# Kernel optimization log

Hardware: AMD Instinct MI355X
Metric: run time of the kernel (lower is better)

The kernel has to match this reference:

```python
import jax, jax.numpy as jnp
import numpy as np

N = 100000   # nodes per type
E = 500000   # edges per edge type
HID = 128    # hidden_channels
H = 4        # heads
D = HID // H # head dim = 32
L = 2        # layers
T = 2        # node types: 0=user, 1=item
R = 2        # edge types: 0=user->item, 1=item->user


def setup_inputs() -> dict:
    key = jax.random.key(0)
    ks = jax.random.split(key, 16)
    s = jnp.float32(0.05)
    f32 = jnp.float32
    return {
        "x_user": jax.random.normal(ks[0], (N, HID), f32),
        "x_item": jax.random.normal(ks[1], (N, HID), f32),
        "W_in": jax.random.normal(ks[2], (T, HID, HID), f32) * s,
        "b_in": jnp.zeros((T, HID), f32),
        "Wk": jax.random.normal(ks[3], (L, T, HID, HID), f32) * s,
        "bk": jnp.zeros((L, T, HID), f32),
        "Wq": jax.random.normal(ks[4], (L, T, HID, HID), f32) * s,
        "bq": jnp.zeros((L, T, HID), f32),
        "Wv": jax.random.normal(ks[5], (L, T, HID, HID), f32) * s,
        "bv": jnp.zeros((L, T, HID), f32),
        "a_rel": jax.random.normal(ks[6], (L, R, H, D, D), f32) * s,
        "m_rel": jax.random.normal(ks[7], (L, R, H, D, D), f32) * s,
        "p_rel": jnp.ones((L, R, H), f32),
        "Wo": jax.random.normal(ks[8], (L, T, HID, HID), f32) * s,
        "bo": jnp.zeros((L, T, HID), f32),
        "skip": jnp.zeros((L, T), f32),
        "edge_ui": jax.random.randint(ks[9], (2, E), 0, N, dtype=jnp.int32),
        "edge_iu": jax.random.randint(ks[10], (2, E), 0, N, dtype=jnp.int32),
    }


def _seg_softmax(logits, seg, n):
    # numerically stable softmax over edges grouped by destination node
    m = jax.ops.segment_max(logits, seg, num_segments=n)            # [N,H]
    m = jnp.where(jnp.isfinite(m), m, jnp.float32(0.0))
    e = jnp.exp(logits - m[seg])                                    # [E,H]
    z = jax.ops.segment_sum(e, seg, num_segments=n)                 # [N,H]
    return e / (z[seg] + jnp.float32(1e-16))


def reference(x_user, x_item, W_in, b_in, Wk, bk, Wq, bq, Wv, bv,
              a_rel, m_rel, p_rel, Wo, bo, skip, edge_ui, edge_iu):
    scale = jnp.float32(1.0 / np.sqrt(D))
    # per-node-type input linear + relu (lin_dict)
    h = [jax.nn.relu(x_user @ W_in[0] + b_in[0]),
         jax.nn.relu(x_item @ W_in[1] + b_in[1])]
    # (edge_type_id, src_type, dst_type, edge_index)
    etypes = [(0, 0, 1, edge_ui), (1, 1, 0, edge_iu)]
    for l in range(L):
        k = [(h[t] @ Wk[l, t] + bk[l, t]).reshape(N, H, D) for t in range(T)]
        q = [(h[t] @ Wq[l, t] + bq[l, t]).reshape(N, H, D) for t in range(T)]
        v = [(h[t] @ Wv[l, t] + bv[l, t]).reshape(N, H, D) for t in range(T)]
        agg = [jnp.zeros((N, H, D), h[0].dtype) for _ in range(T)]
        for r, st, dt, e in etypes:
            src, dst = e[0], e[1]
            # relation-specific transforms applied on node table (N < E)
            k_r = jnp.einsum('nhd,hde->nhe', k[st], a_rel[l, r])
            v_r = jnp.einsum('nhd,hde->nhe', v[st], m_rel[l, r])
            logits = jnp.sum(q[dt][dst] * k_r[src], axis=-1) * p_rel[l, r] * scale  # [E,H]
            alpha = _seg_softmax(logits, dst, N)                                    # [E,H]
            msg = alpha[:, :, None] * v_r[src]                                      # [E,H,D]
            agg[dt] = agg[dt] + jax.ops.segment_sum(msg, dst, num_segments=N)
        h_new = []
        for t in range(T):
            out = agg[t].reshape(N, HID)
            a = jax.nn.gelu(out, approximate=False) @ Wo[l, t] + bo[l, t]
            beta = jax.nn.sigmoid(skip[l, t])
            hn = beta * a + (1.0 - beta) * h[t]
            if l > 0:  # model-level residual (i > 0 in torch code)
                hn = hn + h[t]
            h_new.append(hn)
        h = h_new
    return jnp.stack(h)  # [T, N, HID]
```

## Files before the change

kernel.cpp:

```cpp
#include <hip/hip_runtime.h>
#include <stdint.h>
#include <stdio.h>

#define NN 100000
#define NE 500000
#define HID 128
#define NH 4
#define HD 32
#define LL 2
#define SCANB 1024
#define NB ((NN + SCANB - 1) / SCANB)

typedef unsigned short u16;
typedef unsigned char u8;
typedef unsigned int u32;
typedef __attribute__((ext_vector_type(8))) short bfrag;
typedef __attribute__((ext_vector_type(4))) float f32x4;
typedef __attribute__((ext_vector_type(2))) float f32x2;

__device__ __forceinline__ float b2f(u32 lo16) {
  union { u32 u; float f; } c; c.u = lo16; return c.f;
}
__device__ __forceinline__ u16 f2b(float f) {
  union { float f; u32 u; } c; c.f = f;
  u32 u = c.u;
  u32 r = (u + 0x7FFFu + ((u >> 16) & 1u)) >> 16;
  return (u16)r;
}
__device__ __forceinline__ float geluf(float x) {
  return 0.5f * x * (1.0f + erff(x * 0.70710678118654752f));
}
__device__ __forceinline__ void up8(uint4 a, float* f) {
  f[0] = b2f(a.x << 16); f[1] = b2f(a.x & 0xFFFF0000u);
  f[2] = b2f(a.y << 16); f[3] = b2f(a.y & 0xFFFF0000u);
  f[4] = b2f(a.z << 16); f[5] = b2f(a.z & 0xFFFF0000u);
  f[6] = b2f(a.w << 16); f[7] = b2f(a.w & 0xFFFF0000u);
}

__global__ __launch_bounds__(256) void csr_count(const int* __restrict__ e0,
                                                 const int* __restrict__ e1,
                                                 int* __restrict__ deg) {
  int r = blockIdx.y;
  const int* edges = r ? e1 : e0;
  int e = blockIdx.x * 256 + threadIdx.x;
  if (e < NE) atomicAdd(&deg[(size_t)r * NN + edges[NE + e]], 1);
}

__global__ __launch_bounds__(SCANB) void scan1(const int* __restrict__ deg,
                                               int* __restrict__ rp,
                                               int* __restrict__ bsum) {
  __shared__ int ls[SCANB];
  int r = blockIdx.y;
  int t = threadIdx.x;
  int g = blockIdx.x * SCANB + t;
  int v = (g < NN) ? deg[(size_t)r * NN + g] : 0;
  ls[t] = v;
  __syncthreads();
#pragma unroll
  for (int off = 1; off < SCANB; off <<= 1) {
    int u = (t >= off) ? ls[t - off] : 0;
    __syncthreads();
    ls[t] += u;
    __syncthreads();
  }
  if (g < NN) rp[(size_t)r * (NN + 1) + g] = ls[t] - v;
  if (t == SCANB - 1) bsum[r * NB + blockIdx.x] = ls[t];
}

__global__ __launch_bounds__(128) void scan2(const int* __restrict__ bsum,
                                             int* __restrict__ boff) {
  __shared__ int ls[128];
  int r = blockIdx.y;
  int t = threadIdx.x;
  int v = (t < NB) ? bsum[r * NB + t] : 0;
  ls[t] = v;
  __syncthreads();
#pragma unroll
  for (int off = 1; off < 128; off <<= 1) {
    int u = (t >= off) ? ls[t - off] : 0;
    __syncthreads();
    ls[t] += u;
    __syncthreads();
  }
  if (t < NB) boff[r * NB + t] = ls[t] - v;
}

__global__ __launch_bounds__(SCANB) void scan3(int* __restrict__ rp,
                                               int* __restrict__ cursor,
                                               const int* __restrict__ boff) {
  int r = blockIdx.y;
  int g = blockIdx.x * SCANB + threadIdx.x;
  if (g < NN) {
    int v = rp[(size_t)r * (NN + 1) + g] + boff[r * NB + blockIdx.x];
    rp[(size_t)r * (NN + 1) + g] = v;
    cursor[(size_t)r * NN + g] = v;
  }
  if (g == 0) rp[(size_t)r * (NN + 1) + NN] = NE;
}

__global__ __launch_bounds__(256) void csr_fill(const int* __restrict__ e0,
                                                const int* __restrict__ e1,
                                                int* __restrict__ cursor,
                                                int* __restrict__ s0,
                                                int* __restrict__ s1) {
  int r = blockIdx.y;
  const int* edges = r ? e1 : e0;
  int* srcs = r ? s1 : s0;
  int e = blockIdx.x * 256 + threadIdx.x;
  if (e < NE) {
    int pos = atomicAdd(&cursor[(size_t)r * NN + edges[NE + e]], 1);
    srcs[pos] = edges[e];
  }
}

__global__ __launch_bounds__(256) void hist_deg(const int* __restrict__ rp,
                                                int* __restrict__ hist) {
  __shared__ int lh[64];
  int r = blockIdx.y;
  if (threadIdx.x < 64) lh[threadIdx.x] = 0;
  __syncthreads();
  int d = blockIdx.x * 256 + threadIdx.x;
  if (d < NN) {
    const int* rowptr = rp + (size_t)r * (NN + 1);
    int dg = rowptr[d + 1] - rowptr[d];
    atomicAdd(&lh[dg < 63 ? dg : 63], 1);
  }
  __syncthreads();
  if (threadIdx.x < 64 && lh[threadIdx.x])
    atomicAdd(&hist[r * 64 + threadIdx.x], lh[threadIdx.x]);
}

__global__ __launch_bounds__(64) void scan_hist(const int* __restrict__ hist,
                                                int* __restrict__ hcur) {
  __shared__ int ls[64];
  int r = blockIdx.y;
  int t = threadIdx.x;
  int v = hist[r * 64 + t];
  ls[t] = v;
  __syncthreads();
#pragma unroll
  for (int off = 1; off < 64; off <<= 1) {
    int u = (t >= off) ? ls[t - off] : 0;
    __syncthreads();
    ls[t] += u;
    __syncthreads();
  }
  hcur[r * 64 + t] = ls[t] - v;
}

__global__ __launch_bounds__(256) void scatter_deg(const int* __restrict__ rp,
                                                   int* __restrict__ hcur,
                                                   int* __restrict__ o0,
                                                   int* __restrict__ o1) {
  __shared__ int lh[64];
  __shared__ int lbase[64];
  int r = blockIdx.y;
  int* order = r ? o1 : o0;
  if (threadIdx.x < 64) lh[threadIdx.x] = 0;
  __syncthreads();
  int d = blockIdx.x * 256 + threadIdx.x;
  int dg = 0, rank = 0;
  if (d < NN) {
    const int* rowptr = rp + (size_t)r * (NN + 1);
    dg = rowptr[d + 1] - rowptr[d];
    if (dg > 63) dg = 63;
    rank = atomicAdd(&lh[dg], 1);
  }
  __syncthreads();
  if (threadIdx.x < 64)
    lbase[threadIdx.x] = lh[threadIdx.x] ? atomicAdd(&hcur[r * 64 + threadIdx.x], lh[threadIdx.x]) : 0;
  __syncthreads();
  if (d < NN) order[lbase[dg] + rank] = d;
}

__global__ __launch_bounds__(256) void prep_wT(const float* __restrict__ src, size_t srcStride,
                                               u16* __restrict__ dst, size_t dstStride,
                                               const float* __restrict__ bsrc, int bsStride,
                                               float* __restrict__ bdst, int bdStride,
                                               const float* __restrict__ p_rel_q) {
  int m = blockIdx.y;
  const float* S = src + (size_t)m * srcStride;
  u16* D = dst + (size_t)m * dstStride;
  int idx = blockIdx.x * 256 + threadIdx.x;
  int k = idx >> 7, n = idx & 127;
  float v = S[idx];
  if (p_rel_q != nullptr) {
    int l = m >> 1, t = m & 1;
    v *= p_rel_q[((l << 1) | (1 - t)) * NH + (n >> 5)] * 0.17677669529663687f;
  }
  D[(size_t)n * HID + k] = f2b(v);
  if (bsrc != nullptr && blockIdx.x == 0 && threadIdx.x < HID) {
    int col = threadIdx.x;
    float bvv = bsrc[(size_t)m * bsStride + col];
    if (p_rel_q != nullptr) {
      int l = m >> 1, t = m & 1;
      bvv *= p_rel_q[((l << 1) | (1 - t)) * NH + (col >> 5)] * 0.17677669529663687f;
    }
    bdst[(size_t)m * bdStride + col] = bvv;
  }
}

__global__ __launch_bounds__(256) void combine_all(
    const float* __restrict__ Wk, const float* __restrict__ bk,
    const float* __restrict__ Wv, const float* __restrict__ bv,
    const float* __restrict__ a_rel, const float* __restrict__ m_rel,
    u16* __restrict__ wqkvT, float* __restrict__ bqkv) {
  int l = blockIdx.z;
  int t = blockIdx.y >> 1, which = blockIdx.y & 1;
  const float* W  = (which == 0 ? Wk : Wv) + (size_t)(l * 2 + t) * HID * HID;
  const float* b  = (which == 0 ? bk : bv) + (size_t)(l * 2 + t) * HID;
  const float* Ar = (which == 0 ? a_rel : m_rel) + (size_t)(l * 2 + t) * NH * HD * HD;
  u16* Wd = wqkvT + ((size_t)(l * 2 + t) * 3 + 1 + which) * HID * HID;
  float* bd = bqkv + ((size_t)(l * 2 + t) * 3 + 1 + which) * HID;
  int idx = blockIdx.x * 256 + threadIdx.x;
  int i = idx >> 7, col = idx & 127;
  int h = col >> 5, e = col & 31;
  {
    const float* ap = Ar + h * HD * HD + e;
    const float* wp = W + (size_t)i * HID + h * HD;
    float s = 0.f;
#pragma unroll
    for (int d = 0; d < HD; ++d) s += wp[d] * ap[d * HD];
    Wd[(size_t)col * HID + i] = f2b(s);
  }
  if (blockIdx.x == 0 && threadIdx.x < HID) {
    int col2 = threadIdx.x, h2 = col2 >> 5, e2 = col2 & 31;
    const float* ap = Ar + h2 * HD * HD + e2;
    const float* bp = b + h2 * HD;
    float s = 0.f;
#pragma unroll
    for (int d = 0; d < HD; ++d) s += bp[d] * ap[d * HD];
    bd[col2] = s;
  }
}

__global__ __launch_bounds__(256) void qkv_gemm(
    const u16* __restrict__ h0, const u16* __restrict__ h1,
    const u16* __restrict__ WT,
    const float* __restrict__ bias,
    u16* __restrict__ q0, u16* __restrict__ q1,
    u8* __restrict__ k0, u8* __restrict__ k1,
    u8* __restrict__ v0, u8* __restrict__ v1, int gb) {
  __shared__ __align__(16) u16 sW[3 * HID * HID];
  const int t = blockIdx.x >= gb;
  const int bx = t ? blockIdx.x - gb : blockIdx.x;
  const u16* A = t ? h1 : h0;
  const u16* Wg = WT + (size_t)t * 3 * HID * HID;
  const float* bs = bias + (size_t)t * 3 * HID;
  u16* Oq = t ? q1 : q0;
  u8* Ok = t ? k1 : k0;
  u8* Ov = t ? v1 : v0;

  const int lane = threadIdx.x & 63;
  const int wid = threadIdx.x >> 6;
  const int l16 = lane & 15, g = lane >> 4;
  const int rbase = bx * 128 + wid * 32;

  bfrag af[2][4];
  int rowA[2];
#pragma unroll
  for (int rt = 0; rt < 2; ++rt) {
    int row = rbase + rt * 16 + l16;
    rowA[rt] = row;
    int rl = row < NN ? row : NN - 1;
    const bfrag* ap = (const bfrag*)(A + (size_t)rl * HID);
#pragma unroll
    for (int ks = 0; ks < 4; ++ks) af[rt][ks] = ap[ks * 4 + g];
  }

#pragma unroll
  for (int m = 0; m < 3; ++m) {
#pragma unroll
    for (int j = 0; j < 8; ++j) {
      int ins = wid * 8 + j;
      int o16 = ins * 64 + lane;
      int row = o16 >> 4, ch = o16 & 15;
      const u16* src = Wg + (size_t)m * HID * HID + (size_t)row * HID + ((ch ^ (row & 7)) << 3);
      u16* dst = sW + (size_t)m * HID * HID + (size_t)ins * 512;
      __builtin_amdgcn_global_load_lds(
          (const __attribute__((address_space(1))) unsigned int*)src,
          (__attribute__((address_space(3))) unsigned int*)dst, 16, 0, 0);
    }
  }
  __syncthreads();

#pragma unroll
  for (int m = 0; m < 3; ++m) {
    f32x4 acc[2][8];
#pragma unroll
    for (int rt = 0; rt < 2; ++rt)
#pragma unroll
      for (int ct = 0; ct < 8; ++ct) acc[rt][ct] = (f32x4){0.f, 0.f, 0.f, 0.f};
#pragma unroll
    for (int ct = 0; ct < 8; ++ct) {
      int row = ct * 16 + l16;
      bfrag wf[4];
#pragma unroll
      for (int ks = 0; ks < 4; ++ks)
        wf[ks] = *(const bfrag*)&sW[(size_t)m * HID * HID + (size_t)row * HID +
                                    (((ks * 4 + g) ^ (row & 7)) << 3)];
#pragma unroll
      for (int ks = 0; ks < 4; ++ks)
#pragma unroll
        for (int rt = 0; rt < 2; ++rt)
          acc[rt][ct] = __builtin_amdgcn_mfma_f32_16x16x32_bf16(wf[ks], af[rt][ks],
                                                                acc[rt][ct], 0, 0, 0);
    }
#pragma unroll
    for (int rt = 0; rt < 2; ++rt) {
      int row = rowA[rt];
      if (row >= NN) continue;
#pragma unroll
      for (int ct = 0; ct < 8; ++ct) {
        int nc = ct * 16 + g * 4;
        const float4 bb = *(const float4*)(bs + m * HID + nc);
        float o0 = acc[rt][ct][0] + bb.x;
        float o1 = acc[rt][ct][1] + bb.y;
        float o2 = acc[rt][ct][2] + bb.z;
        float o3 = acc[rt][ct][3] + bb.w;
        if (m == 0) {
          u32 lo = (u32)f2b(o0) | ((u32)f2b(o1) << 16);
          u32 hi = (u32)f2b(o2) | ((u32)f2b(o3) << 16);
          *(uint2*)(Oq + (size_t)row * HID + nc) = make_uint2(lo, hi);
        } else {
          u8* O8 = (m == 1) ? Ok : Ov;
          u32 pk = __builtin_amdgcn_cvt_pk_fp8_f32(o0, o1, 0u, false);
          pk = __builtin_amdgcn_cvt_pk_fp8_f32(o2, o3, pk, true);
          *(u32*)(O8 + (size_t)row * HID + nc) = pk;
        }
      }
    }
  }
}

template <int NMAT, bool RELU, bool SKIP, bool FP8KV, bool AF32>
__global__ __launch_bounds__(256) void mfgemm(
    const void* __restrict__ A0, const void* __restrict__ A1, int M, int gb,
    const u16* __restrict__ WT, size_t wtStride,
    const float* __restrict__ bias, size_t biasStride,
    u16* __restrict__ O00, u16* __restrict__ O01, u16* __restrict__ O02,
    u16* __restrict__ O10, u16* __restrict__ O11, u16* __restrict__ O12,
    float* __restrict__ Of0, float* __restrict__ Of1,
    const u16* __restrict__ hp0, const u16* __restrict__ hp1,
    const float* __restrict__ skipP, int resflag) {
  __shared__ __align__(16) u16 sW[HID * HID];
  const int t = blockIdx.x >= gb;
  const int bx = t ? blockIdx.x - gb : blockIdx.x;
  const void* A = t ? A1 : A0;
  const u16* Wg = WT + (size_t)t * wtStride;
  const float* bs = bias + (size_t)t * biasStride;
  u16* Os[3];
  Os[0] = t ? O10 : O00; Os[1] = t ? O11 : O01; Os[2] = t ? O12 : O02;
  float* Of = t ? Of1 : Of0;
  const u16* hprev = t ? hp1 : hp0;

  const int lane = threadIdx.x & 63;
  const int wid = threadIdx.x >> 6;
  const int l16 = lane & 15, g = lane >> 4;
  const int rbase = bx * 128 + wid * 32;

  float beta = 0.f;
  if (SKIP) beta = 1.f / (1.f + __expf(-skipP[t]));

  auto stageW = [&](int m) {
    const u16* Wm = Wg + (size_t)m * HID * HID;
#pragma unroll
    for (int j = 0; j < 8; ++j) {
      int ins = wid * 8 + j;
      int o16 = ins * 64 + lane;
      int row = o16 >> 4, ch = o16 & 15;
      const u16* src = Wm + (size_t)row * HID + ((ch ^ (row & 7)) << 3);
      u16* dst = sW + (size_t)ins * 512;
      __builtin_amdgcn_global_load_lds(
          (const __attribute__((address_space(1))) unsigned int*)src,
          (__attribute__((address_space(3))) unsigned int*)dst, 16, 0, 0);
    }
  };

  bfrag af[2][4];
  int rowA[2];
#pragma unroll
  for (int rt = 0; rt < 2; ++rt) {
    int row = rbase + rt * 16 + l16;
    rowA[rt] = row;
    int rl = row < M ? row : M - 1;
    if (AF32) {
      const float* apf = (const float*)A + (size_t)rl * HID;
#pragma unroll
      for (int ks = 0; ks < 4; ++ks) {
        float4 u0 = *(const float4*)(apf + (ks * 4 + g) * 8);
        float4 u1 = *(const float4*)(apf + (ks * 4 + g) * 8 + 4);
        union { u16 s[8]; bfrag b; } pk;
        pk.s[0] = f2b(u0.x); pk.s[1] = f2b(u0.y); pk.s[2] = f2b(u0.z); pk.s[3] = f2b(u0.w);
        pk.s[4] = f2b(u1.x); pk.s[5] = f2b(u1.y); pk.s[6] = f2b(u1.z); pk.s[7] = f2b(u1.w);
        af[rt][ks] = pk.b;
      }
    } else {
      const bfrag* ap = (const bfrag*)A + (size_t)rl * (HID / 8);
#pragma unroll
      for (int ks = 0; ks < 4; ++ks) af[rt][ks] = ap[ks * 4 + g];
    }
  }

  stageW(0);
  __syncthreads();

#pragma unroll
  for (int m = 0; m < NMAT; ++m) {
    f32x4 acc[2][8];
#pragma unroll
    for (int rt = 0; rt < 2; ++rt)
#pragma unroll
      for (int ct = 0; ct < 8; ++ct) acc[rt][ct] = (f32x4){0.f, 0.f, 0.f, 0.f};
#pragma unroll
    for (int ct = 0; ct < 8; ++ct) {
      int row = ct * 16 + l16;
      bfrag wf[4];
#pragma unroll
      for (int ks = 0; ks < 4; ++ks)
        wf[ks] = *(const bfrag*)&sW[(size_t)row * HID + (((ks * 4 + g) ^ (row & 7)) << 3)];
#pragma unroll
      for (int ks = 0; ks < 4; ++ks)
#pragma unroll
        for (int rt = 0; rt < 2; ++rt)
          acc[rt][ct] = __builtin_amdgcn_mfma_f32_16x16x32_bf16(wf[ks], af[rt][ks],
                                                                acc[rt][ct], 0, 0, 0);
    }
    if (m + 1 < NMAT) {
      __syncthreads();
      stageW(m + 1);
    }
    u16* Ob = Os[m];
#pragma unroll
    for (int rt = 0; rt < 2; ++rt) {
      int row = rowA[rt];
      if (row >= M) continue;
#pragma unroll
      for (int ct = 0; ct < 8; ++ct) {
        int nc = ct * 16 + g * 4;
        const float4 bb = *(const float4*)(bs + m * HID + nc);
        float o0 = acc[rt][ct][0] + bb.x;
        float o1 = acc[rt][ct][1] + bb.y;
        float o2 = acc[rt][ct][2] + bb.z;
        float o3 = acc[rt][ct][3] + bb.w;
        if (RELU) {
          o0 = fmaxf(o0, 0.f); o1 = fmaxf(o1, 0.f);
          o2 = fmaxf(o2, 0.f); o3 = fmaxf(o3, 0.f);
        }
        if (SKIP) {
          uint2 hh2 = *(const uint2*)(hprev + (size_t)row * HID + nc);
          float h0 = b2f(hh2.x << 16), h1 = b2f(hh2.x & 0xFFFF0000u);
          float h2 = b2f(hh2.y << 16), h3 = b2f(hh2.y & 0xFFFF0000u);
          o0 = beta * o0 + (1.f - beta) * h0;
          o1 = beta * o1 + (1.f - beta) * h1;
          o2 = beta * o2 + (1.f - beta) * h2;
          o3 = beta * o3 + (1.f - beta) * h3;
          if (resflag) { o0 += h0; o1 += h1; o2 += h2; o3 += h3; }
        }
        if (FP8KV && m >= 1) {
          u32 pk = __builtin_amdgcn_cvt_pk_fp8_f32(o0, o1, 0u, false);
          pk = __builtin_amdgcn_cvt_pk_fp8_f32(o2, o3, pk, true);
          *(u32*)((u8*)Ob + (size_t)row * HID + nc) = pk;
        } else {
          if (Ob != nullptr) {
            u32 lo = (u32)f2b(o0) | ((u32)f2b(o1) << 16);
            u32 hi = (u32)f2b(o2) | ((u32)f2b(o3) << 16);
            *(uint2*)(Ob + (size_t)row * HID + nc) = make_uint2(lo, hi);
          }
          if (NMAT == 1 && Of != nullptr) {
            *(float4*)(Of + (size_t)row * HID + nc) = make_float4(o0, o1, o2, o3);
          }
        }
      }
    }
    if (m + 1 < NMAT) __syncthreads();
  }
}

__global__ __launch_bounds__(256) void agg_csr(
    const int* __restrict__ rp0, const int* __restrict__ ss0, const int* __restrict__ od0,
    const u16* __restrict__ q0, const u8* __restrict__ k0,
    const u8* __restrict__ v0, u16* __restrict__ o0,
    const int* __restrict__ rp1, const int* __restrict__ ss1, const int* __restrict__ od1,
    const u16* __restrict__ q1, const u8* __restrict__ k1,
    const u8* __restrict__ v1, u16* __restrict__ o1, int agb) {
  const int r = blockIdx.x >= agb;
  const int bx = r ? blockIdx.x - agb : blockIdx.x;
  int i = bx * 256 + threadIdx.x;
  if (i >= NN * NH) return;
  const int* rowptr = r ? rp1 : rp0;
  const int* srcs = r ? ss1 : ss0;
  const int* order = r ? od1 : od0;
  const u16* qT = r ? q1 : q0;
  const u8* kT = r ? k1 : k0;
  const u8* vT = r ? v1 : v0;
  u16* aggb = r ? o1 : o0;

  int dst = order[i >> 2], h = i & 3;
  float qv[HD];
  {
    const uint4* qp = (const uint4*)(qT + (size_t)dst * HID + h * HD);
#pragma unroll
    for (int j = 0; j < 4; ++j) up8(qp[j], qv + j * 8);
  }
  float acc[HD];
#pragma unroll
  for (int j = 0; j < HD; ++j) acc[j] = 0.f;
  float z = 0.f;
  int b = rowptr[dst], e2 = rowptr[dst + 1];
  for (int idx = b; idx < e2; ++idx) {
    int src = srcs[idx];
    const uint4* kp = (const uint4*)(kT + (size_t)src * HID + h * HD);
    const uint4* vp = (const uint4*)(vT + (size_t)src * HID + h * HD);
    uint4 ka0 = kp[0], ka1 = kp[1];
    uint4 va0 = vp[0], va1 = vp[1];
    u32 kw[8] = {ka0.x, ka0.y, ka0.z, ka0.w, ka1.x, ka1.y, ka1.z, ka1.w};
    u32 vw[8] = {va0.x, va0.y, va0.z, va0.w, va1.x, va1.y, va1.z, va1.w};
    float s = 0.f;
#pragma unroll
    for (int j = 0; j < 8; ++j) {
      f32x2 p0 = __builtin_amdgcn_cvt_pk_f32_fp8(kw[j], false);
      f32x2 p1 = __builtin_amdgcn_cvt_pk_f32_fp8(kw[j], true);
      s += qv[4 * j] * p0.x + qv[4 * j + 1] * p0.y + qv[4 * j + 2] * p1.x + qv[4 * j + 3] * p1.y;
    }
    s = fminf(s, 60.f);
    float ev = __expf(s);
    z += ev;
#pragma unroll
    for (int j = 0; j < 8; ++j) {
      f32x2 p0 = __builtin_amdgcn_cvt_pk_f32_fp8(vw[j], false);
      f32x2 p1 = __builtin_amdgcn_cvt_pk_f32_fp8(vw[j], true);
      acc[4 * j] += ev * p0.x; acc[4 * j + 1] += ev * p0.y;
      acc[4 * j + 2] += ev * p1.x; acc[4 * j + 3] += ev * p1.y;
    }
  }
  float inv = 1.f / (z + 1e-16f);
  u16* ap = aggb + (size_t)dst * HID + h * HD;
  u32 w[16];
#pragma unroll
  for (int j = 0; j < 16; ++j) {
    float a0 = geluf(acc[2 * j] * inv);
    float a1 = geluf(acc[2 * j + 1] * inv);
    w[j] = (u32)f2b(a0) | ((u32)f2b(a1) << 16);
  }
#pragma unroll
  for (int j = 0; j < 4; ++j)
    *(uint4*)(ap + j * 8) = make_uint4(w[4 * j], w[4 * j + 1], w[4 * j + 2], w[4 * j + 3]);
}

extern "C" void kernel_launch(void* const* d_in, const int* in_sizes, int n_in,
                              void* d_out, int out_size, void* d_ws, size_t ws_size,
                              hipStream_t stream) {
  const float* x_user = (const float*)d_in[0];
  const float* x_item = (const float*)d_in[1];
  const float* W_in = (const float*)d_in[2];
  const float* b_in = (const float*)d_in[3];
  const float* Wk = (const float*)d_in[4];
  const float* bk = (const float*)d_in[5];
  const float* Wq = (const float*)d_in[6];
  const float* bq = (const float*)d_in[7];
  const float* Wv = (const float*)d_in[8];
  const float* bv = (const float*)d_in[9];
  const float* a_rel = (const float*)d_in[10];
  const float* m_rel = (const float*)d_in[11];
  const float* p_rel = (const float*)d_in[12];
  const float* Wo = (const float*)d_in[13];
  const float* bo = (const float*)d_in[14];
  const float* skipP = (const float*)d_in[15];
  const int* edge_ui = (const int*)d_in[16];
  const int* edge_iu = (const int*)d_in[17];
  float* out = (float*)d_out;

  char* p = (char*)d_ws;
  auto take = [&](size_t bytes) {
    void* r = (void*)p;
    p += (bytes + 255) & ~(size_t)255;
    return r;
  };
  size_t nodeB = (size_t)NN * HID * sizeof(u16);
  size_t node8 = (size_t)NN * HID;
  u16* hb[2] = {(u16*)take(nodeB), (u16*)take(nodeB)};
  u16* qb[2] = {(u16*)take(nodeB), (u16*)take(nodeB)};
  u8* kb[2] = {(u8*)take(node8), (u8*)take(node8)};
  u8* vb[2] = {(u8*)take(node8), (u8*)take(node8)};
  u16* aggb[2] = {(u16*)take(nodeB), (u16*)take(nodeB)};
  int* deg2   = (int*)take((size_t)2 * NN * 4);
  int* cur2   = (int*)take((size_t)2 * NN * 4);
  int* bsum2  = (int*)take((size_t)2 * NB * 4);
  int* boff2  = (int*)take((size_t)2 * NB * 4);
  int* hist2  = (int*)take((size_t)2 * 64 * 4);
  int* hcur2  = (int*)take((size_t)2 * 64 * 4);
  int* rp2    = (int*)take((size_t)2 * (NN + 1) * 4);
  int* srcs[2]  = {(int*)take((size_t)NE * 4), (int*)take((size_t)NE * 4)};
  int* order[2] = {(int*)take((size_t)NN * 4), (int*)take((size_t)NN * 4)};
  u16* winT  = (u16*)take((size_t)2 * HID * HID * 2);
  u16* woT   = (u16*)take((size_t)4 * HID * HID * 2);
  u16* wqkvT = (u16*)take((size_t)2 * 2 * 3 * HID * HID * 2);
  float* bqkv = (float*)take((size_t)2 * 2 * 3 * HID * 4);
  size_t used = (size_t)(p - (char*)d_ws);
  if (used > ws_size) {
    fprintf(stderr, "HGT kernel: workspace too small: need %zu, have %zu\n", used, ws_size);
    return;
  }

  const int GB = (NN + 127) / 128;
  const int EB = (NE + 255) / 256;
  const int DB = (NN + 255) / 256;
  dim3 blk(256);

  hipMemsetAsync(deg2, 0, (size_t)2 * NN * 4, stream);
  csr_count<<<dim3(EB, 2), blk, 0, stream>>>(edge_ui, edge_iu, deg2);
  scan1<<<dim3(NB, 2), SCANB, 0, stream>>>(deg2, rp2, bsum2);
  scan2<<<dim3(1, 2), 128, 0, stream>>>(bsum2, boff2);
  scan3<<<dim3(NB, 2), SCANB, 0, stream>>>(rp2, cur2, boff2);
  csr_fill<<<dim3(EB, 2), blk, 0, stream>>>(edge_ui, edge_iu, cur2, srcs[0], srcs[1]);
  hipMemsetAsync(hist2, 0, 2 * 64 * 4, stream);
  hist_deg<<<dim3(DB, 2), blk, 0, stream>>>(rp2, hist2);
  scan_hist<<<dim3(1, 2), 64, 0, stream>>>(hist2, hcur2);
  scatter_deg<<<dim3(DB, 2), blk, 0, stream>>>(rp2, hcur2, order[0], order[1]);
  int* rowptr[2] = {rp2, rp2 + (NN + 1)};

  prep_wT<<<dim3(64, 2), blk, 0, stream>>>(W_in, HID * HID, winT, HID * HID,
                                           nullptr, 0, nullptr, 0, nullptr);
  prep_wT<<<dim3(64, 4), blk, 0, stream>>>(Wo, HID * HID, woT, HID * HID,
                                           nullptr, 0, nullptr, 0, nullptr);
  prep_wT<<<dim3(64, 4), blk, 0, stream>>>(Wq, HID * HID, wqkvT, 3 * HID * HID,
                                           bq, HID, bqkv, 3 * HID, p_rel);
  combine_all<<<dim3(64, 4, 2), blk, 0, stream>>>(Wk, bk, Wv, bv, a_rel, m_rel,
                                                  wqkvT, bqkv);

  mfgemm<1, true, false, false, true><<<2 * GB, blk, 0, stream>>>(
      x_user, x_item, NN, GB, winT, HID * HID, b_in, HID,
      hb[0], nullptr, nullptr, hb[1], nullptr, nullptr,
      nullptr, nullptr, nullptr, nullptr, nullptr, 0);

  const int AGB = (NN * NH + 255) / 256;
  for (int l = 0; l < LL; ++l) {
    qkv_gemm<<<2 * GB, blk, 0, stream>>>(
        hb[0], hb[1],
        wqkvT + (size_t)l * 2 * 3 * HID * HID,
        bqkv + (size_t)l * 2 * 3 * HID,
        qb[0], qb[1], kb[0], kb[1], vb[0], vb[1], GB);
    agg_csr<<<2 * AGB, blk, 0, stream>>>(
        rowptr[0], srcs[0], order[0], qb[1], kb[0], vb[0], aggb[1],
        rowptr[1], srcs[1], order[1], qb[0], kb[1], vb[1], aggb[0], AGB);
    if (l == 0) {
      mfgemm<1, false, true, false, false><<<2 * GB, blk, 0, stream>>>(
          aggb[0], aggb[1], NN, GB,
          woT, HID * HID, bo, HID,
          hb[0], nullptr, nullptr, hb[1], nullptr, nullptr,
          nullptr, nullptr, hb[0], hb[1], skipP, 0);
    } else {
      mfgemm<1, false, true, false, false><<<2 * GB, blk, 0, stream>>>(
          aggb[0], aggb[1], NN, GB,
          woT + (size_t)2 * HID * HID, HID * HID, bo + 2 * HID, HID,
          nullptr, nullptr, nullptr, nullptr, nullptr, nullptr,
          out, out + (size_t)NN * HID, hb[0], hb[1], skipP + 2, 1);
    }
  }
}
```

Measured before the change: 545.9 us.

## Make QKV GEMM persistent with 512-thread blocks and prefetched A tiles

The QKV projection kernel becomes persistent: a fixed grid of 128 blocks per node type, each with 512 threads, loops over 256-row chunks. The 96KB weight tile is loaded into LDS once per block instead of once per 128 rows, and the next chunk's A fragments are prefetched into registers while the current chunk's MFMAs run. This cuts redundant weight loads and launch-tail overhead, at the cost of more register pressure and possibly lower occupancy.

```diff
diff --git a/kernel.cpp b/kernel.cpp
--- a/kernel.cpp
+++ b/kernel.cpp
@@ -10,6 +10,8 @@
 #define LL 2
 #define SCANB 1024
 #define NB ((NN + SCANB - 1) / SCANB)
+#define QSLOT 128
+#define QCHUNKS ((NN + 255) / 256)
 
 typedef unsigned short u16;
 typedef unsigned char u8;
@@ -234,16 +236,16 @@
   }
 }
 
-__global__ __launch_bounds__(256) void qkv_gemm(
+__global__ __launch_bounds__(512) void qkv_gemm(
     const u16* __restrict__ h0, const u16* __restrict__ h1,
     const u16* __restrict__ WT,
     const float* __restrict__ bias,
     u16* __restrict__ q0, u16* __restrict__ q1,
     u8* __restrict__ k0, u8* __restrict__ k1,
-    u8* __restrict__ v0, u8* __restrict__ v1, int gb) {
+    u8* __restrict__ v0, u8* __restrict__ v1) {
   __shared__ __align__(16) u16 sW[3 * HID * HID];
-  const int t = blockIdx.x >= gb;
-  const int bx = t ? blockIdx.x - gb : blockIdx.x;
+  const int t = blockIdx.x >= QSLOT;
+  const int slot = t ? blockIdx.x - QSLOT : blockIdx.x;
   const u16* A = t ? h1 : h0;
   const u16* Wg = WT + (size_t)t * 3 * HID * HID;
   const float* bs = bias + (size_t)t * 3 * HID;
@@ -254,14 +256,12 @@
   const int lane = threadIdx.x & 63;
   const int wid = threadIdx.x >> 6;
   const int l16 = lane & 15, g = lane >> 4;
-  const int rbase = bx * 128 + wid * 32;
-
+
+  int c = slot;
   bfrag af[2][4];
-  int rowA[2];
 #pragma unroll
   for (int rt = 0; rt < 2; ++rt) {
-    int row = rbase + rt * 16 + l16;
-    rowA[rt] = row;
+    int row = c * 256 + wid * 32 + rt * 16 + l16;
     int rl = row < NN ? row : NN - 1;
     const bfrag* ap = (const bfrag*)(A + (size_t)rl * HID);
 #pragma unroll
@@ -271,8 +271,8 @@
 #pragma unroll
   for (int m = 0; m < 3; ++m) {
 #pragma unroll
-    for (int j = 0; j < 8; ++j) {
-      int ins = wid * 8 + j;
+    for (int j = 0; j < 4; ++j) {
+      int ins = wid * 4 + j;
       int o16 = ins * 64 + lane;
       int row = o16 >> 4, ch = o16 & 15;
       const u16* src = Wg + (size_t)m * HID * HID + (size_t)row * HID + ((ch ^ (row & 7)) << 3);
@@ -284,52 +284,74 @@
   }
   __syncthreads();
 
-#pragma unroll
-  for (int m = 0; m < 3; ++m) {
-    f32x4 acc[2][8];
-#pragma unroll
-    for (int rt = 0; rt < 2; ++rt)
-#pragma unroll
-      for (int ct = 0; ct < 8; ++ct) acc[rt][ct] = (f32x4){0.f, 0.f, 0.f, 0.f};
-#pragma unroll
-    for (int ct = 0; ct < 8; ++ct) {
-      int row = ct * 16 + l16;
-      bfrag wf[4];
-#pragma unroll
-      for (int ks = 0; ks < 4; ++ks)
-        wf[ks] = *(const bfrag*)&sW[(size_t)m * HID * HID + (size_t)row * HID +
-                                    (((ks * 4 + g) ^ (row & 7)) << 3)];
-#pragma unroll
-      for (int ks = 0; ks < 4; ++ks)
-#pragma unroll
-        for (int rt = 0; rt < 2; ++rt)
-          acc[rt][ct] = __builtin_amdgcn_mfma_f32_16x16x32_bf16(wf[ks], af[rt][ks],
-                                                                acc[rt][ct], 0, 0, 0);
-    }
-#pragma unroll
-    for (int rt = 0; rt < 2; ++rt) {
-      int row = rowA[rt];
-      if (row >= NN) continue;
+  while (true) {
+    const int cn = c + QSLOT;
+    bfrag afn[2][4];
+    if (cn < QCHUNKS) {
+#pragma unroll
+      for (int rt = 0; rt < 2; ++rt) {
+        int row = cn * 256 + wid * 32 + rt * 16 + l16;
+        int rl = row < NN ? row : NN - 1;
+        const bfrag* ap = (const bfrag*)(A + (size_t)rl * HID);
+#pragma unroll
+        for (int ks = 0; ks < 4; ++ks) afn[rt][ks] = ap[ks * 4 + g];
+      }
+    }
+
+    const int rbase = c * 256 + wid * 32;
+#pragma unroll
+    for (int m = 0; m < 3; ++m) {
+      f32x4 acc[2][8];
+#pragma unroll
+      for (int rt = 0; rt < 2; ++rt)
+#pragma unroll
+        for (int ct = 0; ct < 8; ++ct) acc[rt][ct] = (f32x4){0.f, 0.f, 0.f, 0.f};
 #pragma unroll
       for (int ct = 0; ct < 8; ++ct) {
-        int nc = ct * 16 + g * 4;
-        const float4 bb = *(const float4*)(bs + m * HID + nc);
-        float o0 = acc[rt][ct][0] + bb.x;
-        float o1 = acc[rt][ct][1] + bb.y;
-        float o2 = acc[rt][ct][2] + bb.z;
-        float o3 = acc[rt][ct][3] + bb.w;
-        if (m == 0) {
-          u32 lo = (u32)f2b(o0) | ((u32)f2b(o1) << 16);
-          u32 hi = (u32)f2b(o2) | ((u32)f2b(o3) << 16);
-          *(uint2*)(Oq + (size_t)row * HID + nc) = make_uint2(lo, hi);
-        } else {
-          u8* O8 = (m == 1) ? Ok : Ov;
-          u32 pk = __builtin_amdgcn_cvt_pk_fp8_f32(o0, o1, 0u, false);
-          pk = __builtin_amdgcn_cvt_pk_fp8_f32(o2, o3, pk, true);
-          *(u32*)(O8 + (size_t)row * HID + nc) = pk;
+        int row = ct * 16 + l16;
+        bfrag wf[4];
+#pragma unroll
+        for (int ks = 0; ks < 4; ++ks)
+          wf[ks] = *(const bfrag*)&sW[(size_t)m * HID * HID + (size_t)row * HID +
+                                      (((ks * 4 + g) ^ (row & 7)) << 3)];
+#pragma unroll
+        for (int ks = 0; ks < 4; ++ks)
+#pragma unroll
+          for (int rt = 0; rt < 2; ++rt)
+            acc[rt][ct] = __builtin_amdgcn_mfma_f32_16x16x32_bf16(wf[ks], af[rt][ks],
+                                                                  acc[rt][ct], 0, 0, 0);
+      }
+#pragma unroll
+      for (int rt = 0; rt < 2; ++rt) {
+        int row = rbase + rt * 16 + l16;
+        if (row >= NN) continue;
+#pragma unroll
+        for (int ct = 0; ct < 8; ++ct) {
+          int nc = ct * 16 + g * 4;
+          const float4 bb = *(const float4*)(bs + m * HID + nc);
+          float o0 = acc[rt][ct][0] + bb.x;
+          float o1 = acc[rt][ct][1] + bb.y;
+          float o2 = acc[rt][ct][2] + bb.z;
+          float o3 = acc[rt][ct][3] + bb.w;
+          if (m == 0) {
+            u32 lo = (u32)f2b(o0) | ((u32)f2b(o1) << 16);
+            u32 hi = (u32)f2b(o2) | ((u32)f2b(o3) << 16);
+            *(uint2*)(Oq + (size_t)row * HID + nc) = make_uint2(lo, hi);
+          } else {
+            u8* O8 = (m == 1) ? Ok : Ov;
+            u32 pk = __builtin_amdgcn_cvt_pk_fp8_f32(o0, o1, 0u, false);
+            pk = __builtin_amdgcn_cvt_pk_fp8_f32(o2, o3, pk, true);
+            *(u32*)(O8 + (size_t)row * HID + nc) = pk;
+          }
         }
       }
     }
+    if (cn >= QCHUNKS) break;
+#pragma unroll
+    for (int rt = 0; rt < 2; ++rt)
+#pragma unroll
+      for (int ks = 0; ks < 4; ++ks) af[rt][ks] = afn[rt][ks];
+    c = cn;
   }
 }
 
@@ -636,11 +658,11 @@
 
   const int AGB = (NN * NH + 255) / 256;
   for (int l = 0; l < LL; ++l) {
-    qkv_gemm<<<2 * GB, blk, 0, stream>>>(
+    qkv_gemm<<<2 * QSLOT, dim3(512), 0, stream>>>(
         hb[0], hb[1],
         wqkvT + (size_t)l * 2 * 3 * HID * HID,
         bqkv + (size_t)l * 2 * 3 * HID,
-        qb[0], qb[1], kb[0], kb[1], vb[0], vb[1], GB);
+        qb[0], qb[1], kb[0], kb[1], vb[0], vb[1]);
     agg_csr<<<2 * AGB, blk, 0, stream>>>(
         rowptr[0], srcs[0], order[0], qb[1], kb[0], vb[0], aggb[1],
         rowptr[1], srcs[1], order[1], qb[0], kb[1], vb[1], aggb[0], AGB);
```

New measurement: 828.4 us. +51.7%, slower.
